# Kernel optimization log

Measured on AMD Instinct MI355X. Metric: run time of the kernel, lower is better.

## Reference

```python
import jax, jax.numpy as jnp
import numpy as np

B, C, H, W = 16, 3, 384, 1280
EPS = 1e-7


def setup_inputs() -> dict:
    key = jax.random.key(0)
    k1, k2, k3, k4 = jax.random.split(key, 4)
    source_image = jax.random.normal(k1, (B, C, H, W), jnp.float32)
    depth_map = jax.random.uniform(k2, (B, 1, H, W), jnp.float32, minval=0.1, maxval=80.0)
    pose = 0.05 * jax.random.normal(k3, (B, 6), jnp.float32)
    # realistic KITTI-style pinhole intrinsics, per-batch mild perturbation
    base = jnp.array([[0.58 * W, 0.0, 0.5 * W],
                      [0.0, 1.92 * H, 0.5 * H],
                      [0.0, 0.0, 1.0]], jnp.float32)
    noise = 1.0 + 0.01 * jax.random.normal(k4, (B, 3, 3), jnp.float32)
    intrinsic = base[None] * noise  # zero entries stay zero -> invertible
    return {"source_image": source_image, "depth_map": depth_map,
            "pose": pose, "intrinsic": intrinsic}


def rot_from_axisangle(aa):
    # aa: [B,3] -> [B,3,3] (Rodrigues)
    theta = jnp.linalg.norm(aa, axis=-1, keepdims=True)  # [B,1]
    axis = aa / (theta + EPS)
    c = jnp.cos(theta)
    s = jnp.sin(theta)
    t = 1.0 - c
    x, y, z = axis[:, 0:1], axis[:, 1:2], axis[:, 2:3]
    row0 = jnp.concatenate([t * x * x + c, t * x * y - s * z, t * z * x + s * y], axis=1)
    row1 = jnp.concatenate([t * x * y + s * z, t * y * y + c, t * y * z - s * x], axis=1)
    row2 = jnp.concatenate([t * z * x - s * y, t * y * z + s * x, t * z * z + c], axis=1)
    return jnp.stack([row0, row1, row2], axis=1)  # [B,3,3]


def bilinear_grid_sample(img, gx, gy):
    # img: [B,C,H,W]; gx,gy: [B,H,W] in [-1,1]; align_corners=True, padding zeros
    Bc, Cc, Hc, Wc = img.shape
    x = (gx + 1.0) * 0.5 * (Wc - 1)
    y = (gy + 1.0) * 0.5 * (Hc - 1)
    x0 = jnp.floor(x)
    y0 = jnp.floor(y)
    x1 = x0 + 1.0
    y1 = y0 + 1.0
    wx1 = x - x0
    wx0 = 1.0 - wx1
    wy1 = y - y0
    wy0 = 1.0 - wy1
    imgf = img.reshape(Bc, Cc, Hc * Wc)

    def gather(xi, yi):
        inb = ((xi >= 0) & (xi <= Wc - 1) & (yi >= 0) & (yi <= Hc - 1)).astype(img.dtype)
        xc = jnp.clip(xi, 0, Wc - 1).astype(jnp.int32)
        yc = jnp.clip(yi, 0, Hc - 1).astype(jnp.int32)
        idx = (yc * Wc + xc).reshape(Bc, 1, -1)
        vals = jnp.take_along_axis(imgf, jnp.broadcast_to(idx, (Bc, Cc, idx.shape[-1])), axis=2)
        return vals.reshape(Bc, Cc, Hc, Wc) * inb[:, None]

    out = (gather(x0, y0) * (wx0 * wy0)[:, None]
           + gather(x1, y0) * (wx1 * wy0)[:, None]
           + gather(x0, y1) * (wx0 * wy1)[:, None]
           + gather(x1, y1) * (wx1 * wy1)[:, None])
    return out


def reference(source_image, depth_map, pose, intrinsic):
    Bb, _, Hh, Ww = depth_map.shape
    # pixel grid, homogeneous [H,W,3] = (x, y, 1)
    ys, xs = jnp.meshgrid(jnp.arange(Hh, dtype=depth_map.dtype),
                          jnp.arange(Ww, dtype=depth_map.dtype), indexing='ij')
    pix = jnp.stack([xs, ys, jnp.ones_like(xs)], axis=-1)  # [H,W,3]
    # backproject: K^{-1} @ pix * depth
    inv_K = jnp.linalg.inv(intrinsic)  # [B,3,3]
    cam = jnp.einsum('bij,hwj->bhwi', inv_K, pix)  # [B,H,W,3]
    frustum = cam * jnp.transpose(depth_map, (0, 2, 3, 1))  # [B,H,W,3]
    # rigid transform
    R = rot_from_axisangle(pose[:, :3])  # [B,3,3]
    t = pose[:, 3:]  # [B,3]
    points = jnp.einsum('bij,bhwj->bhwi', R, frustum) + t[:, None, None, :]
    # project with K
    coord = jnp.einsum('bij,bhwj->bhwi', intrinsic, points)  # [B,H,W,3]
    z = coord[..., 2] + EPS
    px = coord[..., 0] / z
    py = coord[..., 1] / z
    gx = px / (Ww - 1) * 2.0 - 1.0
    gy = py / (Hh - 1) * 2.0 - 1.0
    return bilinear_grid_sample(source_image, gx, gy)
```

## Files before the change

kernel.cpp:

```cpp
#include <hip/hip_runtime.h>

#define B_ 16
#define C_ 3
#define H_ 384
#define W_ 1280
#define HW_ (H_*W_)
#define EPS_ 1e-7f

typedef float v2f __attribute__((ext_vector_type(2)));

__device__ __forceinline__ v2f load2(const float* p) {
  v2f r;
  __builtin_memcpy(&r, p, 8);
  return r;
}

__device__ __forceinline__ void mat3mul(const float* A, const float* Bm, float* C) {
  #pragma unroll
  for (int i = 0; i < 3; i++)
    #pragma unroll
    for (int j = 0; j < 3; j++)
      C[i*3+j] = A[i*3+0]*Bm[0*3+j] + A[i*3+1]*Bm[1*3+j] + A[i*3+2]*Bm[2*3+j];
}

__device__ void compute_MT(const float* __restrict__ pose,
                           const float* __restrict__ intr,
                           int b, float* M, float* T)
{
  float K[9];
  #pragma unroll
  for (int i = 0; i < 9; i++) K[i] = intr[b*9 + i];
  float aa0 = pose[b*6 + 0], aa1 = pose[b*6 + 1], aa2 = pose[b*6 + 2];
  float t0  = pose[b*6 + 3], t1  = pose[b*6 + 4], t2  = pose[b*6 + 5];

  float theta = sqrtf(aa0*aa0 + aa1*aa1 + aa2*aa2);
  float invn  = 1.0f / (theta + EPS_);
  float x = aa0*invn, y = aa1*invn, z = aa2*invn;
  float c = cosf(theta), s = sinf(theta), t = 1.0f - c;
  float R[9] = {
    t*x*x + c,   t*x*y - s*z, t*z*x + s*y,
    t*x*y + s*z, t*y*y + c,   t*y*z - s*x,
    t*z*x - s*y, t*y*z + s*x, t*z*z + c
  };

  float a = K[0], bb = K[1], cc = K[2];
  float d = K[3], e  = K[4], f  = K[5];
  float g = K[6], h  = K[7], ii = K[8];
  float A0 = e*ii - f*h, A1 = f*g - d*ii, A2 = d*h - e*g;
  float id = 1.0f / (a*A0 + bb*A1 + cc*A2);
  float iK[9] = {
    A0*id, (cc*h - bb*ii)*id, (bb*f - cc*e)*id,
    A1*id, (a*ii - cc*g)*id,  (cc*d - a*f)*id,
    A2*id, (bb*g - a*h)*id,   (a*e  - bb*d)*id
  };

  float KR[9];
  mat3mul(K, R, KR);
  mat3mul(KR, iK, M);
  T[0] = K[0]*t0 + K[1]*t1 + K[2]*t2;
  T[1] = K[3]*t0 + K[4]*t1 + K[5]*t2;
  T[2] = K[6]*t0 + K[7]*t1 + K[8]*t2;
}

__global__ __launch_bounds__(256) void warp_kernel(
    const float* __restrict__ src,
    const float* __restrict__ depth,
    const float* __restrict__ pose,
    const float* __restrict__ intr,
    float* __restrict__ out)
{
  __shared__ float sp[12];
  int b = blockIdx.y;
  if (threadIdx.x == 0) {
    float M[9], T[3];
    compute_MT(pose, intr, b, M, T);
    #pragma unroll
    for (int i = 0; i < 9; i++) sp[i] = M[i];
    #pragma unroll
    for (int i = 0; i < 3; i++) sp[9 + i] = T[i];
  }
  __syncthreads();
  float m00 = sp[0], m01 = sp[1], m02 = sp[2];
  float m10 = sp[3], m11 = sp[4], m12 = sp[5];
  float m20 = sp[6], m21 = sp[7], m22 = sp[8];
  float T0  = sp[9], T1  = sp[10], T2 = sp[11];

  int p = blockIdx.x * 256 + threadIdx.x;
  int j = p % W_;
  int i = p / W_;

  float d  = depth[(size_t)b * HW_ + p];
  float xf = (float)j, yf = (float)i;

  float cx = (m00*xf + m01*yf + m02)*d + T0;
  float cy = (m10*xf + m11*yf + m12)*d + T1;
  float cz = (m20*xf + m21*yf + m22)*d + T2;
  float inv = 1.0f / (cz + EPS_);
  float px = cx * inv;
  float py = cy * inv;

  float x0f = floorf(px), y0f = floorf(py);
  float x1f = x0f + 1.0f, y1f = y0f + 1.0f;
  float wx1 = px - x0f, wx0 = 1.0f - wx1;
  float wy1 = py - y0f, wy0 = 1.0f - wy1;

  float mx0 = (x0f >= 0.0f && x0f <= (float)(W_-1)) ? 1.0f : 0.0f;
  float mx1 = (x1f >= 0.0f && x1f <= (float)(W_-1)) ? 1.0f : 0.0f;
  float my0 = (y0f >= 0.0f && y0f <= (float)(H_-1)) ? 1.0f : 0.0f;
  float my1 = (y1f >= 0.0f && y1f <= (float)(H_-1)) ? 1.0f : 0.0f;

  int xc0 = (int)fminf(fmaxf(x0f, 0.0f), (float)(W_-1));
  int xc1 = (int)fminf(fmaxf(x1f, 0.0f), (float)(W_-1));
  int yc0 = (int)fminf(fmaxf(y0f, 0.0f), (float)(H_-1));
  int yc1 = (int)fminf(fmaxf(y1f, 0.0f), (float)(H_-1));

  float w00 = wx0*wy0*mx0*my0;
  float w01 = wx1*wy0*mx1*my0;
  float w10 = wx0*wy1*mx0*my1;
  float w11 = wx1*wy1*mx1*my1;

  int base = xc0 < (W_-2) ? xc0 : (W_-2);
  bool s0 = (xc0 == base);
  bool s1 = (xc1 == base + 1);
  float wax = (s0 ? w00 : 0.0f) + (s1 ? 0.0f : w01);
  float way = (s0 ? 0.0f : w00) + (s1 ? w01 : 0.0f);
  float wbx = (s0 ? w10 : 0.0f) + (s1 ? 0.0f : w11);
  float wby = (s0 ? 0.0f : w10) + (s1 ? w11 : 0.0f);

  int rb0 = yc0*W_ + base;
  int rb1 = yc1*W_ + base;

  size_t sb = (size_t)b * C_ * HW_;
  size_t op = (size_t)p;
  const float* s0p = src + sb;
  const float* s1p = s0p + HW_;
  const float* s2p = s1p + HW_;

  v2f a0 = load2(s0p + rb0);
  v2f b0 = load2(s0p + rb1);
  v2f a1 = load2(s1p + rb0);
  v2f b1 = load2(s1p + rb1);
  v2f a2 = load2(s2p + rb0);
  v2f b2 = load2(s2p + rb1);

  float v0 = a0.x*wax + a0.y*way + b0.x*wbx + b0.y*wby;
  float v1 = a1.x*wax + a1.y*way + b1.x*wbx + b1.y*wby;
  float v2 = a2.x*wax + a2.y*way + b2.x*wbx + b2.y*wby;

  __builtin_nontemporal_store(v0, &out[sb + op]);
  __builtin_nontemporal_store(v1, &out[sb + HW_ + op]);
  __builtin_nontemporal_store(v2, &out[sb + 2*(size_t)HW_ + op]);
}

extern "C" void kernel_launch(void* const* d_in, const int* in_sizes, int n_in,
                              void* d_out, int out_size, void* d_ws, size_t ws_size,
                              hipStream_t stream) {
  const float* src   = (const float*)d_in[0];
  const float* depth = (const float*)d_in[1];
  const float* pose  = (const float*)d_in[2];
  const float* intr  = (const float*)d_in[3];
  float* out = (float*)d_out;

  dim3 grid(HW_ / 256, B_);
  warp_kernel<<<grid, 256, 0, stream>>>(src, depth, pose, intr, out);
}
```

Measured before the change: 238.9 us.

## Remap blocks so each XCD owns two batches and process two pixels per thread

Switches to a 1D grid where the low three bits of the block index pick an XCD, and each XCD is assigned two whole batch images. This keeps the gathered source image in that XCD's L2 instead of spreading it across all eight. Each thread now handles two pixels (p and p+256), which halves the block count and the per-block matrix setup, and gives more independent loads in flight. The mapping assumes round-robin dispatch of blocks to XCDs and uses more registers per thread.

```diff
diff --git a/kernel.cpp b/kernel.cpp
--- a/kernel.cpp
+++ b/kernel.cpp
@@ -6,6 +6,7 @@
 #define W_ 1280
 #define HW_ (H_*W_)
 #define EPS_ 1e-7f
+#define QB_ 960
 
 typedef float v2f __attribute__((ext_vector_type(2)));
 
@@ -62,34 +63,17 @@
   T[2] = K[6]*t0 + K[7]*t1 + K[8]*t2;
 }
 
-__global__ __launch_bounds__(256) void warp_kernel(
-    const float* __restrict__ src,
-    const float* __restrict__ depth,
-    const float* __restrict__ pose,
-    const float* __restrict__ intr,
-    float* __restrict__ out)
+struct Tap { int rb0, rb1; float wax, way, wbx, wby; };
+
+__device__ __forceinline__ Tap make_tap(
+    int p, float d,
+    float m00, float m01, float m02,
+    float m10, float m11, float m12,
+    float m20, float m21, float m22,
+    float T0, float T1, float T2)
 {
-  __shared__ float sp[12];
-  int b = blockIdx.y;
-  if (threadIdx.x == 0) {
-    float M[9], T[3];
-    compute_MT(pose, intr, b, M, T);
-    #pragma unroll
-    for (int i = 0; i < 9; i++) sp[i] = M[i];
-    #pragma unroll
-    for (int i = 0; i < 3; i++) sp[9 + i] = T[i];
-  }
-  __syncthreads();
-  float m00 = sp[0], m01 = sp[1], m02 = sp[2];
-  float m10 = sp[3], m11 = sp[4], m12 = sp[5];
-  float m20 = sp[6], m21 = sp[7], m22 = sp[8];
-  float T0  = sp[9], T1  = sp[10], T2 = sp[11];
-
-  int p = blockIdx.x * 256 + threadIdx.x;
   int j = p % W_;
   int i = p / W_;
-
-  float d  = depth[(size_t)b * HW_ + p];
   float xf = (float)j, yf = (float)i;
 
   float cx = (m00*xf + m01*yf + m02)*d + T0;
@@ -122,34 +106,81 @@
   int base = xc0 < (W_-2) ? xc0 : (W_-2);
   bool s0 = (xc0 == base);
   bool s1 = (xc1 == base + 1);
-  float wax = (s0 ? w00 : 0.0f) + (s1 ? 0.0f : w01);
-  float way = (s0 ? 0.0f : w00) + (s1 ? w01 : 0.0f);
-  float wbx = (s0 ? w10 : 0.0f) + (s1 ? 0.0f : w11);
-  float wby = (s0 ? 0.0f : w10) + (s1 ? w11 : 0.0f);
 
-  int rb0 = yc0*W_ + base;
-  int rb1 = yc1*W_ + base;
+  Tap t;
+  t.wax = (s0 ? w00 : 0.0f) + (s1 ? 0.0f : w01);
+  t.way = (s0 ? 0.0f : w00) + (s1 ? w01 : 0.0f);
+  t.wbx = (s0 ? w10 : 0.0f) + (s1 ? 0.0f : w11);
+  t.wby = (s0 ? 0.0f : w10) + (s1 ? w11 : 0.0f);
+  t.rb0 = yc0*W_ + base;
+  t.rb1 = yc1*W_ + base;
+  return t;
+}
+
+__global__ __launch_bounds__(256) void warp_kernel(
+    const float* __restrict__ src,
+    const float* __restrict__ depth,
+    const float* __restrict__ pose,
+    const float* __restrict__ intr,
+    float* __restrict__ out)
+{
+  __shared__ float sp[12];
+  int n   = blockIdx.x;
+  int xcd = n & 7;
+  int s   = n >> 3;
+  int bo  = (s >= QB_) ? 1 : 0;
+  int q   = s - bo * QB_;
+  int b   = (xcd << 1) | bo;
+
+  if (threadIdx.x == 0) {
+    float M[9], T[3];
+    compute_MT(pose, intr, b, M, T);
+    #pragma unroll
+    for (int i = 0; i < 9; i++) sp[i] = M[i];
+    #pragma unroll
+    for (int i = 0; i < 3; i++) sp[9 + i] = T[i];
+  }
+  __syncthreads();
+  float m00 = sp[0], m01 = sp[1], m02 = sp[2];
+  float m10 = sp[3], m11 = sp[4], m12 = sp[5];
+  float m20 = sp[6], m21 = sp[7], m22 = sp[8];
+  float T0  = sp[9], T1  = sp[10], T2 = sp[11];
+
+  int p0 = q * 512 + threadIdx.x;
+  int p1 = p0 + 256;
+
+  size_t db = (size_t)b * HW_;
+  float d0 = depth[db + p0];
+  float d1 = depth[db + p1];
+
+  Tap A = make_tap(p0, d0, m00,m01,m02, m10,m11,m12, m20,m21,m22, T0,T1,T2);
+  Tap Bt= make_tap(p1, d1, m00,m01,m02, m10,m11,m12, m20,m21,m22, T0,T1,T2);
 
   size_t sb = (size_t)b * C_ * HW_;
-  size_t op = (size_t)p;
-  const float* s0p = src + sb;
-  const float* s1p = s0p + HW_;
-  const float* s2p = s1p + HW_;
+  const float* c0 = src + sb;
+  const float* c1 = c0 + HW_;
+  const float* c2 = c1 + HW_;
 
-  v2f a0 = load2(s0p + rb0);
-  v2f b0 = load2(s0p + rb1);
-  v2f a1 = load2(s1p + rb0);
-  v2f b1 = load2(s1p + rb1);
-  v2f a2 = load2(s2p + rb0);
-  v2f b2 = load2(s2p + rb1);
+  v2f A00 = load2(c0 + A.rb0),  A01 = load2(c0 + A.rb1);
+  v2f A10 = load2(c1 + A.rb0),  A11 = load2(c1 + A.rb1);
+  v2f A20 = load2(c2 + A.rb0),  A21 = load2(c2 + A.rb1);
+  v2f B00 = load2(c0 + Bt.rb0), B01 = load2(c0 + Bt.rb1);
+  v2f B10 = load2(c1 + Bt.rb0), B11 = load2(c1 + Bt.rb1);
+  v2f B20 = load2(c2 + Bt.rb0), B21 = load2(c2 + Bt.rb1);
 
-  float v0 = a0.x*wax + a0.y*way + b0.x*wbx + b0.y*wby;
-  float v1 = a1.x*wax + a1.y*way + b1.x*wbx + b1.y*wby;
-  float v2 = a2.x*wax + a2.y*way + b2.x*wbx + b2.y*wby;
+  float vA0 = A00.x*A.wax + A00.y*A.way + A01.x*A.wbx + A01.y*A.wby;
+  float vA1 = A10.x*A.wax + A10.y*A.way + A11.x*A.wbx + A11.y*A.wby;
+  float vA2 = A20.x*A.wax + A20.y*A.way + A21.x*A.wbx + A21.y*A.wby;
+  float vB0 = B00.x*Bt.wax + B00.y*Bt.way + B01.x*Bt.wbx + B01.y*Bt.wby;
+  float vB1 = B10.x*Bt.wax + B10.y*Bt.way + B11.x*Bt.wbx + B11.y*Bt.wby;
+  float vB2 = B20.x*Bt.wax + B20.y*Bt.way + B21.x*Bt.wbx + B21.y*Bt.wby;
 
-  __builtin_nontemporal_store(v0, &out[sb + op]);
-  __builtin_nontemporal_store(v1, &out[sb + HW_ + op]);
-  __builtin_nontemporal_store(v2, &out[sb + 2*(size_t)HW_ + op]);
+  __builtin_nontemporal_store(vA0, &out[sb + p0]);
+  __builtin_nontemporal_store(vA1, &out[sb + HW_ + p0]);
+  __builtin_nontemporal_store(vA2, &out[sb + 2*(size_t)HW_ + p0]);
+  __builtin_nontemporal_store(vB0, &out[sb + p1]);
+  __builtin_nontemporal_store(vB1, &out[sb + HW_ + p1]);
+  __builtin_nontemporal_store(vB2, &out[sb + 2*(size_t)HW_ + p1]);
 }
 
 extern "C" void kernel_launch(void* const* d_in, const int* in_sizes, int n_in,
@@ -161,6 +192,5 @@
   const float* intr  = (const float*)d_in[3];
   float* out = (float*)d_out;
 
-  dim3 grid(HW_ / 256, B_);
-  warp_kernel<<<grid, 256, 0, stream>>>(src, depth, pose, intr, out);
+  warp_kernel<<<dim3(8 * 2 * QB_), 256, 0, stream>>>(src, depth, pose, intr, out);
 }
```

Result: slower. 254.7 us (+6.6%).
